# Kernel optimization log

Hardware: AMD Instinct MI355X
Metric: run time of the kernel (lower is better)

Reference implementation:

```python
import jax, jax.numpy as jnp
import numpy as np


def _resize_bilinear_ac(x, oh, ow):
    """Bilinear resize with align_corners=True for NCHW input."""
    ih, iw = x.shape[-2], x.shape[-1]
    ys = jnp.linspace(0.0, ih - 1.0, oh)
    xs = jnp.linspace(0.0, iw - 1.0, ow)
    y0 = jnp.floor(ys).astype(jnp.int32)
    y1 = jnp.minimum(y0 + 1, ih - 1)
    wy = (ys - y0).astype(x.dtype)[None, None, :, None]
    x0 = jnp.floor(xs).astype(jnp.int32)
    x1 = jnp.minimum(x0 + 1, iw - 1)
    wx = (xs - x0).astype(x.dtype)[None, None, None, :]
    top = x[:, :, y0, :] * (1 - wy) + x[:, :, y1, :] * wy  # (B,1,oh,iw)
    return top[:, :, :, x0] * (1 - wx) + top[:, :, :, x1] * wx  # (B,1,oh,ow)


def raw_to_rgb_bg(image):
    """Demosaic a (*,1,H,W) bayer raw image, CFA.BG layout (top-left red)."""
    orig_shape = image.shape
    H, W = image.shape[-2], image.shape[-1]
    img = image.reshape(-1, 1, H, W)

    # CFA.BG: red at even rows/cols, blue at odd rows/cols
    r = img[:, :, ::2, ::2]   # (B,1,H/2,W/2)
    b = img[:, :, 1::2, 1::2]
    # rpad=(0,1,0,1): pad right/bottom by 1; bpad=(1,0,1,0): pad left/top by 1 (replicate)
    rpadded = jnp.pad(r, ((0, 0), (0, 0), (0, 1), (0, 1)), mode='edge')
    bpadded = jnp.pad(b, ((0, 0), (0, 0), (1, 0), (1, 0)), mode='edge')

    ru = _resize_bilinear_ac(rpadded, H + 1, W + 1)
    bu = _resize_bilinear_ac(bpadded, H + 1, W + 1)
    # negative padding = crop back to (H, W)
    ru = ru[:, :, :H, :W]      # crop right/bottom
    bu = bu[:, :, 1:, 1:]      # crop left/top

    # green: reflect-pad and apply fixed cross kernel (4-neighbour average)
    gp = jnp.pad(img, ((0, 0), (0, 0), (1, 1), (1, 1)), mode='reflect')
    gu = 0.25 * (gp[:, :, :-2, 1:-1] + gp[:, :, 2:, 1:-1]
                 + gp[:, :, 1:-1, :-2] + gp[:, :, 1:-1, 2:])
    # overwrite known green samples (CFA.BG: green at (even,odd) and (odd,even))
    gu = gu.at[:, :, ::2, 1::2].set(img[:, :, ::2, 1::2])
    gu = gu.at[:, :, 1::2, ::2].set(img[:, :, 1::2, ::2])

    ru = ru.reshape(orig_shape)
    gu = gu.reshape(orig_shape)
    bu = bu.reshape(orig_shape)
    return jnp.concatenate([ru, gu, bu], axis=-3)


def setup_inputs() -> dict:
    key = jax.random.key(0)
    image = jax.random.uniform(key, (8, 1, 2048, 2048), dtype=jnp.float32)
    return {"image": image}


def reference(image):
    return raw_to_rgb_bg(image)
```

## Files before the change

### kernel.cpp

```cpp
#include <hip/hip_runtime.h>


#define HH 2048
#define WW 2048

struct Row { float l; float4 c; float r; };

__device__ __forceinline__ Row load_row(const float* __restrict__ p, int x0) {
    Row o;
    int xl = (x0 == 0) ? 1 : x0 - 1;
    int xr = (x0 + 4 > WW - 2) ? (WW - 2) : x0 + 4;
    o.l = p[xl];
    o.c = *(const float4*)(p + x0);
    o.r = p[xr];
    return o;
}

__global__ __launch_bounds__(256) void demosaic_bg_kernel(const float* __restrict__ in,
                                                          float* __restrict__ out) {
    const int strips_per_row = WW / 4;
    int gid = blockIdx.x * blockDim.x + threadIdx.x;
    int s = gid & (strips_per_row - 1);
    int t = gid >> 9;
    int yp = t & (HH / 2 - 1);
    int b = t >> 10;
    int y = yp << 1;
    int x0 = s << 2;

    const float* __restrict__ img = in + (size_t)b * HH * WW;

    const int i0 = (y == 0) ? 1 : y - 1;
    const int i3 = (y + 2 > HH - 2) ? (HH - 2) : y + 2;

    Row r0 = load_row(img + (size_t)i0 * WW, x0);
    Row r1 = load_row(img + (size_t)y * WW, x0);
    Row r2 = load_row(img + (size_t)(y + 1) * WW, x0);
    Row r3 = load_row(img + (size_t)i3 * WW, x0);

    float4 Re, Ge, Be;
    Re.x = r1.c.x;
    Ge.x = 0.25f * (r0.c.x + r2.c.x + r1.l + r1.c.y);
    Be.x = 0.25f * (r0.l + r0.c.y + r2.l + r2.c.y);

    Re.y = 0.5f * (r1.c.x + r1.c.z);
    Ge.y = r1.c.y;
    Be.y = 0.5f * (r0.c.y + r2.c.y);

    Re.z = r1.c.z;
    Ge.z = 0.25f * (r0.c.z + r2.c.z + r1.c.y + r1.c.w);
    Be.z = 0.25f * (r0.c.y + r0.c.w + r2.c.y + r2.c.w);

    Re.w = 0.5f * (r1.c.z + r1.r);
    Ge.w = r1.c.w;
    Be.w = 0.5f * (r0.c.w + r2.c.w);

    float4 Ro, Go, Bo;
    Ro.x = 0.5f * (r1.c.x + r3.c.x);
    Go.x = r2.c.x;
    Bo.x = 0.5f * (r2.l + r2.c.y);

    Ro.y = 0.25f * (r1.c.x + r1.c.z + r3.c.x + r3.c.z);
    Go.y = 0.25f * (r1.c.y + r3.c.y + r2.c.x + r2.c.z);
    Bo.y = r2.c.y;

    Ro.z = 0.5f * (r1.c.z + r3.c.z);
    Go.z = r2.c.z;
    Bo.z = 0.5f * (r2.c.y + r2.c.w);

    Ro.w = 0.25f * (r1.c.z + r1.r + r3.c.z + r3.r);
    Go.w = 0.25f * (r1.c.w + r3.c.w + r2.c.z + r2.r);
    Bo.w = r2.c.w;

    const size_t plane = (size_t)HH * WW;
    size_t obase = (size_t)b * 3 * plane + (size_t)y * WW + x0;
    *(float4*)(out + obase)                 = Re;
    *(float4*)(out + obase + WW)            = Ro;
    *(float4*)(out + obase + plane)         = Ge;
    *(float4*)(out + obase + plane + WW)    = Go;
    *(float4*)(out + obase + 2 * plane)     = Be;
    *(float4*)(out + obase + 2 * plane + WW) = Bo;
}

extern "C" void kernel_launch(void* const* d_in, const int* in_sizes, int n_in,
                              void* d_out, int out_size, void* d_ws, size_t ws_size,
                              hipStream_t stream) {
    const float* in = (const float*)d_in[0];
    float* out = (float*)d_out;
    const int threads = 8 * (HH / 2) * (WW / 4);
    dim3 block(256);
    dim3 grid(threads / 256);
    demosaic_bg_kernel<<<grid, block, 0, stream>>>(in, out);
}
```

Baseline: 475.4 us.

## Use wavefront shuffles for halo columns and swizzle block order across XCDs

Replaces the per-thread scalar halo loads (left and right neighbour columns of each row) with __shfl_up/__shfl_down taken from adjacent lanes' float4 loads, so only wavefront-edge lanes issue extra scalar global loads. It also remaps blockIdx so consecutive logical blocks are spread in a strided pattern, which suits the round-robin dispatch of blocks across MI355X XCDs and is meant to improve L2 locality for the shared rows. The kernel is bandwidth bound and the scalar loads mostly hit cache, so the gain may be small, and edge lanes now take divergent branches.

```diff
diff --git a/kernel.cpp b/kernel.cpp
--- a/kernel.cpp
+++ b/kernel.cpp
@@ -4,80 +4,100 @@
 #define HH 2048
 #define WW 2048
 
-struct Row { float l; float4 c; float r; };
-
-__device__ __forceinline__ Row load_row(const float* __restrict__ p, int x0) {
-    Row o;
-    int xl = (x0 == 0) ? 1 : x0 - 1;
-    int xr = (x0 + 4 > WW - 2) ? (WW - 2) : x0 + 4;
-    o.l = p[xl];
-    o.c = *(const float4*)(p + x0);
-    o.r = p[xr];
-    return o;
-}
-
 __global__ __launch_bounds__(256) void demosaic_bg_kernel(const float* __restrict__ in,
                                                           float* __restrict__ out) {
     const int strips_per_row = WW / 4;
-    int gid = blockIdx.x * blockDim.x + threadIdx.x;
+
+    int bid = (int)blockIdx.x;
+    int nb = (bid & 7) * ((int)gridDim.x >> 3) + (bid >> 3);
+    int gid = nb * 256 + (int)threadIdx.x;
+
     int s = gid & (strips_per_row - 1);
     int t = gid >> 9;
     int yp = t & (HH / 2 - 1);
-    int b = t >> 10;
+    int bimg = t >> 10;
     int y = yp << 1;
     int x0 = s << 2;
+    int lane = (int)threadIdx.x & 63;
 
-    const float* __restrict__ img = in + (size_t)b * HH * WW;
+    const float* __restrict__ img = in + (size_t)bimg * HH * WW;
 
     const int i0 = (y == 0) ? 1 : y - 1;
     const int i3 = (y + 2 > HH - 2) ? (HH - 2) : y + 2;
 
-    Row r0 = load_row(img + (size_t)i0 * WW, x0);
-    Row r1 = load_row(img + (size_t)y * WW, x0);
-    Row r2 = load_row(img + (size_t)(y + 1) * WW, x0);
-    Row r3 = load_row(img + (size_t)i3 * WW, x0);
+    const float* pa = img + (size_t)i0 * WW;
+    const float* pb = img + (size_t)y * WW;
+    const float* pc = img + (size_t)(y + 1) * WW;
+    const float* pd = img + (size_t)i3 * WW;
+
+    float4 a = *(const float4*)(pa + x0);
+    float4 b = *(const float4*)(pb + x0);
+    float4 c = *(const float4*)(pc + x0);
+    float4 d = *(const float4*)(pd + x0);
+
+    float la = __shfl_up(a.w, 1);
+    float lb = __shfl_up(b.w, 1);
+    float lc = __shfl_up(c.w, 1);
+    float rb = __shfl_down(b.x, 1);
+    float rc = __shfl_down(c.x, 1);
+    float rd = __shfl_down(d.x, 1);
+
+    if (lane == 0) {
+        if (x0 == 0) {
+            la = a.y; lb = b.y; lc = c.y;
+        } else {
+            la = pa[x0 - 1]; lb = pb[x0 - 1]; lc = pc[x0 - 1];
+        }
+    }
+    if (lane == 63) {
+        if (x0 + 4 > WW - 2) {
+            rb = b.z; rc = c.z; rd = d.z;
+        } else {
+            rb = pb[x0 + 4]; rc = pc[x0 + 4]; rd = pd[x0 + 4];
+        }
+    }
 
     float4 Re, Ge, Be;
-    Re.x = r1.c.x;
-    Ge.x = 0.25f * (r0.c.x + r2.c.x + r1.l + r1.c.y);
-    Be.x = 0.25f * (r0.l + r0.c.y + r2.l + r2.c.y);
+    Re.x = b.x;
+    Ge.x = 0.25f * (a.x + c.x + lb + b.y);
+    Be.x = 0.25f * (la + a.y + lc + c.y);
 
-    Re.y = 0.5f * (r1.c.x + r1.c.z);
-    Ge.y = r1.c.y;
-    Be.y = 0.5f * (r0.c.y + r2.c.y);
+    Re.y = 0.5f * (b.x + b.z);
+    Ge.y = b.y;
+    Be.y = 0.5f * (a.y + c.y);
 
-    Re.z = r1.c.z;
-    Ge.z = 0.25f * (r0.c.z + r2.c.z + r1.c.y + r1.c.w);
-    Be.z = 0.25f * (r0.c.y + r0.c.w + r2.c.y + r2.c.w);
+    Re.z = b.z;
+    Ge.z = 0.25f * (a.z + c.z + b.y + b.w);
+    Be.z = 0.25f * (a.y + a.w + c.y + c.w);
 
-    Re.w = 0.5f * (r1.c.z + r1.r);
-    Ge.w = r1.c.w;
-    Be.w = 0.5f * (r0.c.w + r2.c.w);
+    Re.w = 0.5f * (b.z + rb);
+    Ge.w = b.w;
+    Be.w = 0.5f * (a.w + c.w);
 
     float4 Ro, Go, Bo;
-    Ro.x = 0.5f * (r1.c.x + r3.c.x);
-    Go.x = r2.c.x;
-    Bo.x = 0.5f * (r2.l + r2.c.y);
+    Ro.x = 0.5f * (b.x + d.x);
+    Go.x = c.x;
+    Bo.x = 0.5f * (lc + c.y);
 
-    Ro.y = 0.25f * (r1.c.x + r1.c.z + r3.c.x + r3.c.z);
-    Go.y = 0.25f * (r1.c.y + r3.c.y + r2.c.x + r2.c.z);
-    Bo.y = r2.c.y;
+    Ro.y = 0.25f * (b.x + b.z + d.x + d.z);
+    Go.y = 0.25f * (b.y + d.y + c.x + c.z);
+    Bo.y = c.y;
 
-    Ro.z = 0.5f * (r1.c.z + r3.c.z);
-    Go.z = r2.c.z;
-    Bo.z = 0.5f * (r2.c.y + r2.c.w);
+    Ro.z = 0.5f * (b.z + d.z);
+    Go.z = c.z;
+    Bo.z = 0.5f * (c.y + c.w);
 
-    Ro.w = 0.25f * (r1.c.z + r1.r + r3.c.z + r3.r);
-    Go.w = 0.25f * (r1.c.w + r3.c.w + r2.c.z + r2.r);
-    Bo.w = r2.c.w;
+    Ro.w = 0.25f * (b.z + rb + d.z + rd);
+    Go.w = 0.25f * (b.w + d.w + c.z + rc);
+    Bo.w = c.w;
 
     const size_t plane = (size_t)HH * WW;
-    size_t obase = (size_t)b * 3 * plane + (size_t)y * WW + x0;
-    *(float4*)(out + obase)                 = Re;
-    *(float4*)(out + obase + WW)            = Ro;
-    *(float4*)(out + obase + plane)         = Ge;
-    *(float4*)(out + obase + plane + WW)    = Go;
-    *(float4*)(out + obase + 2 * plane)     = Be;
+    size_t obase = (size_t)bimg * 3 * plane + (size_t)y * WW + x0;
+    *(float4*)(out + obase)                  = Re;
+    *(float4*)(out + obase + WW)             = Ro;
+    *(float4*)(out + obase + plane)          = Ge;
+    *(float4*)(out + obase + plane + WW)     = Go;
+    *(float4*)(out + obase + 2 * plane)      = Be;
     *(float4*)(out + obase + 2 * plane + WW) = Bo;
 }
 
```

New measurement: 485.8 us. 2.2% more time.
